# Optimization experiments

Measured on AMD Instinct MI355X. Metric: run time of the kernel, lower is better.

The kernel has to match this reference:

```python
import jax, jax.numpy as jnp
import numpy as np

NUM_CLASSES = 20
NUM_ANCHORS = 3
STRIDES = (8, 16, 32)
FMP = (320, 160, 80)
TOPK = 100
CONF_THRESH = 0.01
NMS_THRESH = 0.5
ANCHOR_SIZE = np.array([[12, 16], [19, 36], [40, 28], [36, 75], [76, 55], [72, 146],
                        [142, 110], [192, 243], [459, 401]], dtype=np.float32).reshape(3, NUM_ANCHORS, 2)


def make_anchors(level):
    h = w = FMP[level]
    ys, xs = jnp.meshgrid(jnp.arange(h, dtype=jnp.float32), jnp.arange(w, dtype=jnp.float32), indexing='ij')
    xy = jnp.stack([xs, ys], axis=-1).reshape(-1, 1, 2) + 0.5            # [HW,1,2] grid centers
    xy = jnp.broadcast_to(xy, (h * w, NUM_ANCHORS, 2))
    wh = jnp.broadcast_to(jnp.asarray(ANCHOR_SIZE[level]), (h * w, NUM_ANCHORS, 2))
    return jnp.concatenate([xy, wh], axis=-1).reshape(-1, 4)             # [HW*A, 4]


def level_topk(obj, cls, reg, level):
    C = NUM_CLASSES
    # [1, ch, H, W] -> [H*W*A, ch_per_anchor], matching permute(1,2,0).view(-1, .)
    obj = obj[0].transpose(1, 2, 0).reshape(-1, 1)
    cls = cls[0].transpose(1, 2, 0).reshape(-1, C)
    reg = reg[0].transpose(1, 2, 0).reshape(-1, 4)
    anchors = make_anchors(level)
    # decode: ctr = (sigmoid(txy)*3 - 1.5 + grid) * stride ; wh = exp(twh) * anchor_wh
    ctr = (jax.nn.sigmoid(reg[:, :2]) * 3.0 - 1.5 + anchors[:, :2]) * STRIDES[level]
    wh = jnp.exp(reg[:, 2:]) * anchors[:, 2:]
    boxes = jnp.concatenate([ctr - 0.5 * wh, ctr + 0.5 * wh], axis=-1)   # [N, 4] xyxy
    scores = (jax.nn.sigmoid(obj) * jax.nn.sigmoid(cls)).reshape(-1)     # [N*C]
    top_s, top_i = jax.lax.top_k(scores, TOPK)
    anchor_idx = top_i // C
    labels = top_i % C
    return top_s, labels, boxes[anchor_idx], top_s > CONF_THRESH


def nms_fixed(boxes, scores, labels, valid):
    # class-aware greedy NMS on a fixed candidate set; suppressed entries get score 0 / keep False
    K = scores.shape[0]
    order = jnp.argsort(-scores)
    b, s, l, v = boxes[order], scores[order], labels[order], valid[order]
    areas = (b[:, 2] - b[:, 0]) * (b[:, 3] - b[:, 1])
    xx1 = jnp.maximum(b[:, None, 0], b[None, :, 0])
    yy1 = jnp.maximum(b[:, None, 1], b[None, :, 1])
    xx2 = jnp.minimum(b[:, None, 2], b[None, :, 2])
    yy2 = jnp.minimum(b[:, None, 3], b[None, :, 3])
    inter = jnp.maximum(1e-10, xx2 - xx1) * jnp.maximum(1e-10, yy2 - yy1)
    iou = inter / (areas[:, None] + areas[None, :] - inter)
    sup_mat = (iou > NMS_THRESH) & (l[:, None] == l[None, :])            # per-class suppression
    idx = jnp.arange(K)

    def body(i, state):
        suppressed, keep = state
        is_kept = jnp.logical_and(jnp.logical_not(suppressed[i]), v[i])
        keep = keep.at[i].set(is_kept)
        suppressed = suppressed | (is_kept & sup_mat[i] & (idx > i))
        return suppressed, keep

    _, keep = jax.lax.fori_loop(0, K, body, (jnp.zeros(K, bool), jnp.zeros(K, bool)))
    return b, s * keep.astype(s.dtype), l, keep


def setup_inputs() -> dict:
    key = jax.random.key(0)
    ks = jax.random.split(key, 9)
    shapes = {
        'obj0': (1, NUM_ANCHORS, 320, 320), 'cls0': (1, NUM_ANCHORS * NUM_CLASSES, 320, 320), 'reg0': (1, NUM_ANCHORS * 4, 320, 320),
        'obj1': (1, NUM_ANCHORS, 160, 160), 'cls1': (1, NUM_ANCHORS * NUM_CLASSES, 160, 160), 'reg1': (1, NUM_ANCHORS * 4, 160, 160),
        'obj2': (1, NUM_ANCHORS, 80, 80), 'cls2': (1, NUM_ANCHORS * NUM_CLASSES, 80, 80), 'reg2': (1, NUM_ANCHORS * 4, 80, 80),
    }
    return {name: jax.random.normal(k, shp, dtype=jnp.float32)
            for k, (name, shp) in zip(ks, shapes.items())}


def reference(obj0, cls0, reg0, obj1, cls1, reg1, obj2, cls2, reg2):
    levels = [(obj0, cls0, reg0), (obj1, cls1, reg1), (obj2, cls2, reg2)]
    parts = [level_topk(o, c, r, i) for i, (o, c, r) in enumerate(levels)]
    scores = jnp.concatenate([p[0] for p in parts])
    labels = jnp.concatenate([p[1] for p in parts])
    boxes = jnp.concatenate([p[2] for p in parts])
    valid = jnp.concatenate([p[3] for p in parts])
    return nms_fixed(boxes, scores, labels, valid)  # (bboxes[300,4], scores[300], labels[300], keep[300])
```

## Files before the change

### kernel.cpp

```cpp
#include <hip/hip_runtime.h>
#include <stdint.h>

typedef unsigned int u32;
typedef unsigned long long u64;

#define TOPK 100
#define CAP 4096
#define NB 512
#define BINBASE 32000u
#define KAB_BLOCKS 394

__device__ const float ANC[3][3][2] = {
  {{12.f,16.f},{19.f,36.f},{40.f,28.f}},
  {{36.f,75.f},{76.f,55.f},{72.f,146.f}},
  {{142.f,110.f},{192.f,243.f},{459.f,401.f}}
};

__device__ __forceinline__ float sigmoidf_(float x) {
  if (x >= 0.f) return 1.f / (1.f + expf(-x));
  float e = expf(x);
  return e / (1.f + e);
}

__device__ __forceinline__ float fcomp(const float4& v, int q) {
  switch (q) {
    case 0: return v.x;
    case 1: return v.y;
    case 2: return v.z;
    default: return v.w;
  }
}

__global__ __launch_bounds__(256) void kA_scan(
    const float* __restrict__ obj0, const float* __restrict__ cls0,
    const float* __restrict__ obj1, const float* __restrict__ cls1,
    const float* __restrict__ obj2, const float* __restrict__ cls2,
    u32* __restrict__ hist, float* __restrict__ amax)
{
  __shared__ u32 h[NB];
  int tid = threadIdx.x;
  h[tid] = 0; h[tid + 256] = 0;
  __syncthreads();

  int b = blockIdx.x;
  const float *obj, *cls; int P, L, abase; u32 task;
  if (b < 300)      { L=0; obj=obj0; cls=cls0; P=102400; abase=0;      task=(u32)(b*256+tid); }
  else if (b < 375) { L=1; obj=obj1; cls=cls1; P=25600;  abase=307200; task=(u32)((b-300)*256+tid); }
  else              { L=2; obj=obj2; cls=cls2; P=6400;   abase=384000; task=(u32)((b-375)*256+tid); }
  int tpa = P >> 2;
  bool valid = task < (u32)(3*tpa);

  if (valid) {
    int a = (int)(task / (u32)tpa), rem = (int)(task % (u32)tpa);
    int p0 = rem * 4;
    float4 o4 = *(const float4*)(obj + a*P + p0);
    const float* cp = cls + (size_t)(a*20)*P + p0;
    float4 cv[20];
    #pragma unroll
    for (int k = 0; k < 20; ++k) cv[k] = *(const float4*)(cp + (size_t)k*P);
    float4 cm = cv[0];
    #pragma unroll
    for (int k = 1; k < 20; ++k) {
      cm.x = fmaxf(cm.x, cv[k].x); cm.y = fmaxf(cm.y, cv[k].y);
      cm.z = fmaxf(cm.z, cv[k].z); cm.w = fmaxf(cm.w, cv[k].w);
    }
    float4 am4;
    am4.x = sigmoidf_(o4.x) * sigmoidf_(cm.x);
    am4.y = sigmoidf_(o4.y) * sigmoidf_(cm.y);
    am4.z = sigmoidf_(o4.z) * sigmoidf_(cm.z);
    am4.w = sigmoidf_(o4.w) * sigmoidf_(cm.w);
    *(float4*)(amax + abase + a*P + p0) = am4;
    #pragma unroll
    for (int q = 0; q < 4; ++q) {
      u32 bt = __float_as_uint(fcomp(am4, q));
      if (bt >= (BINBASE << 15)) {
        u32 bin = (bt >> 15) - BINBASE;
        if (bin < NB) atomicAdd(&h[bin], 1u);
      }
    }
  }
  __syncthreads();
  if (h[tid])       atomicAdd(&hist[L*NB + tid],       h[tid]);
  if (h[tid + 256]) atomicAdd(&hist[L*NB + tid + 256], h[tid + 256]);
}

__global__ __launch_bounds__(256) void kB_collect(
    const float* __restrict__ obj0, const float* __restrict__ cls0,
    const float* __restrict__ obj1, const float* __restrict__ cls1,
    const float* __restrict__ obj2, const float* __restrict__ cls2,
    const float* __restrict__ amax, const u32* __restrict__ hist,
    u32* __restrict__ cnt, u64* __restrict__ cand)
{
  __shared__ u32 s[NB];
  __shared__ u32 sThr;
  int tid = threadIdx.x;
  int b = blockIdx.x;
  const float *obj, *cls; int P, L, abase; u32 task;
  if (b < 300)      { L=0; obj=obj0; cls=cls0; P=102400; abase=0;      task=(u32)(b*256+tid); }
  else if (b < 375) { L=1; obj=obj1; cls=cls1; P=25600;  abase=307200; task=(u32)((b-300)*256+tid); }
  else              { L=2; obj=obj2; cls=cls2; P=6400;   abase=384000; task=(u32)((b-375)*256+tid); }
  int tpa = P >> 2;
  bool valid = task < (u32)(3*tpa);

  s[tid] = hist[L*NB + tid]; s[tid + 256] = hist[L*NB + tid + 256];
  __syncthreads();
  for (int off = 1; off < NB; off <<= 1) {
    u32 v0 = s[tid]       + ((tid + off < NB)       ? s[tid + off]       : 0u);
    u32 v1 = s[tid + 256] + ((tid + 256 + off < NB) ? s[tid + 256 + off] : 0u);
    __syncthreads();
    s[tid] = v0; s[tid + 256] = v1;
    __syncthreads();
  }
  if (tid == 0 && s[0] < TOPK) sThr = BINBASE << 15;
  {
    int i0 = tid, i1 = tid + 256;
    u32 a0 = s[i0], n0 = (i0 + 1 < NB) ? s[i0 + 1] : 0u;
    if (a0 >= TOPK && n0 < TOPK) sThr = (BINBASE + (u32)i0) << 15;
    u32 a1 = s[i1], n1 = (i1 + 1 < NB) ? s[i1 + 1] : 0u;
    if (a1 >= TOPK && n1 < TOPK) sThr = (BINBASE + (u32)i1) << 15;
  }
  __syncthreads();
  u32 thr = sThr;

  if (valid) {
    int a = (int)(task / (u32)tpa), rem = (int)(task % (u32)tpa);
    int p0 = rem * 4;
    float4 am4 = *(const float4*)(amax + abase + a*P + p0);
    bool any = (__float_as_uint(am4.x) >= thr) | (__float_as_uint(am4.y) >= thr) |
               (__float_as_uint(am4.z) >= thr) | (__float_as_uint(am4.w) >= thr);
    if (any) {
      float4 o4 = *(const float4*)(obj + a*P + p0);
      const float* cp = cls + (size_t)(a*20)*P + p0;
      float4 cv[20];
      #pragma unroll
      for (int k = 0; k < 20; ++k) cv[k] = *(const float4*)(cp + (size_t)k*P);
      #pragma unroll
      for (int q = 0; q < 4; ++q) {
        if (__float_as_uint(fcomp(am4, q)) >= thr) {
          float so = sigmoidf_(fcomp(o4, q));
          int p = p0 + q;
          #pragma unroll
          for (int k = 0; k < 20; ++k) {
            float sc = so * sigmoidf_(fcomp(cv[k], q));
            u32 bits = __float_as_uint(sc);
            if (bits >= thr) {
              u32 pos = atomicAdd(&cnt[L], 1u);
              u32 idx = (u32)(p*60 + a*20 + k);
              if (pos < CAP) cand[L*CAP + pos] = ((u64)bits << 32) | (u64)(0x00FFFFFFu - idx);
            }
          }
        }
      }
    }
  }
}

__global__ __launch_bounds__(256) void kC1_select(
    const float* __restrict__ reg0, const float* __restrict__ reg1, const float* __restrict__ reg2,
    const u64* __restrict__ cand, const u32* __restrict__ cnt,
    u64* __restrict__ selg, float* __restrict__ boxg, float* __restrict__ scg,
    int* __restrict__ lbg, int* __restrict__ vdg)
{
  __shared__ u64 keys[CAP + 4];
  __shared__ u64 selL[TOPK];
  int tid = threadIdx.x;
  int L = blockIdx.x;

  if (tid < TOPK) selL[tid] = 0ull;
  __syncthreads();

  u32 n = cnt[L]; if (n > CAP) n = CAP;
  u32 n4 = (n + 3u) & ~3u;
  for (u32 j = (u32)tid; j < n; j += 256) keys[j] = cand[L*CAP + j];
  if (tid < 4 && n + (u32)tid < n4) keys[n + tid] = 0ull;
  __syncthreads();

  for (u32 j = (u32)tid; j < n; j += 256) {
    u64 kk = keys[j]; int r = 0;
    for (u32 t = 0; t < n4; t += 4) {
      u64 k0 = keys[t], k1 = keys[t+1], k2 = keys[t+2], k3 = keys[t+3];
      r += (k0 > kk) ? 1 : 0; r += (k1 > kk) ? 1 : 0;
      r += (k2 > kk) ? 1 : 0; r += (k3 > kk) ? 1 : 0;
    }
    if (r < TOPK) selL[r] = kk;
  }
  __syncthreads();

  if (tid < TOPK) {
    const float* reg; int Pq, W, stride;
    if (L == 0)      { reg = reg0; Pq = 102400; W = 320; stride = 8; }
    else if (L == 1) { reg = reg1; Pq = 25600;  W = 160; stride = 16; }
    else             { reg = reg2; Pq = 6400;   W = 80;  stride = 32; }
    int g = L*TOPK + tid;
    u64 key = selL[tid];
    selg[g] = key;
    if (key == 0) {
      scg[g] = 0.f; lbg[g] = 0; vdg[g] = 0;
      boxg[g*4+0] = boxg[g*4+1] = boxg[g*4+2] = boxg[g*4+3] = 0.f;
    } else {
      float score = __uint_as_float((u32)(key >> 32));
      u32 i = 0x00FFFFFFu - (u32)(key & 0xFFFFFFFFull);
      int c = (int)(i % 60u), p = (int)(i / 60u);
      int aa = c / 20, k = c % 20;
      int x = p % W, y = p / W;
      float tx = reg[(aa*4+0)*Pq + p], ty = reg[(aa*4+1)*Pq + p];
      float tw = reg[(aa*4+2)*Pq + p], th = reg[(aa*4+3)*Pq + p];
      float cx = (sigmoidf_(tx)*3.f - 1.5f + (float)x + 0.5f) * (float)stride;
      float cy = (sigmoidf_(ty)*3.f - 1.5f + (float)y + 0.5f) * (float)stride;
      float bw = expf(tw) * ANC[L][aa][0];
      float bh = expf(th) * ANC[L][aa][1];
      scg[g] = score; lbg[g] = k; vdg[g] = (score > 0.01f) ? 1 : 0;
      boxg[g*4+0] = cx - 0.5f*bw; boxg[g*4+1] = cy - 0.5f*bh;
      boxg[g*4+2] = cx + 0.5f*bw; boxg[g*4+3] = cy + 0.5f*bh;
    }
  }
}

__global__ __launch_bounds__(1024) void kC2_nms(
    const u64* __restrict__ selg, const float* __restrict__ boxg,
    const float* __restrict__ scg, const int* __restrict__ lbg, const int* __restrict__ vdg,
    float* __restrict__ out)
{
  extern __shared__ uint8_t smem[];
  u64*    mat   = (u64*)(smem);
  float4* ibox4 = (float4*)(smem + 12000);
  float2* iml2  = (float2*)(smem + 16800);
  float*  x1s   = (float*)(smem + 19200);
  float*  y1s   = (float*)(smem + 20400);
  float*  x2s   = (float*)(smem + 21600);
  float*  y2s   = (float*)(smem + 22800);
  float*  sc2   = (float*)(smem + 24000);
  int*    lb2   = (int*)(smem + 25200);
  int*    vd2   = (int*)(smem + 26400);
  u64*    rowAny= (u64*)(smem + 27600);
  u64*    km    = (u64*)(smem + 27648);
  float*  ars   = (float*)(smem + 27696);
  u64*    selAll= (u64*)(smem + 28896);

  int tid = threadIdx.x;
  if (tid < 300) selAll[tid] = selg[tid];
  __syncthreads();

  if (tid < 300) {
    int Lm = tid / TOPK, rr = tid % TOPK;
    u64 kk = selAll[tid];
    int rank = rr;
    #pragma unroll
    for (int Lo = 0; Lo < 3; ++Lo) {
      if (Lo == Lm) continue;
      const u64* arr = selAll + Lo*TOPK;
      bool ge = (Lo < Lm);
      int lo = 0;
      #pragma unroll
      for (int st = 64; st > 0; st >>= 1) {
        int nxt = lo + st;
        if (nxt <= TOPK) {
          u64 v = arr[nxt - 1];
          bool pred = ge ? (v >= kk) : (v > kk);
          if (pred) lo = nxt;
        }
      }
      rank += lo;
    }
    float4 bb = *(const float4*)(boxg + tid*4);
    float x1 = bb.x, y1 = bb.y, x2 = bb.z, y2 = bb.w;
    float ar = (x2 - x1) * (y2 - y1);
    ibox4[rank] = make_float4(x1, y1, x2, y2);
    iml2[rank]  = make_float2(ar, (float)lbg[tid]);
    x1s[rank] = x1; y1s[rank] = y1; x2s[rank] = x2; y2s[rank] = y2; ars[rank] = ar;
    sc2[rank] = scg[tid]; lb2[rank] = lbg[tid]; vd2[rank] = vdg[tid];
  }
  __syncthreads();

  {
    int wave = tid >> 6, lane = tid & 63;
    if (wave < 15) {
      int w = (wave >= 10) ? 4 : (wave >= 6) ? 3 : (wave >= 3) ? 2 : (wave >= 1) ? 1 : 0;
      int ns = w + 1;
      int stripe = wave - ((w*(w+1)) >> 1);
      int j = w*64 + lane;
      bool jv = j < 300;
      float jx1=0.f, jy1=0.f, jx2=0.f, jy2=0.f, jar=0.f; float jlb=-1.f;
      if (jv) { jx1=x1s[j]; jy1=y1s[j]; jx2=x2s[j]; jy2=y2s[j]; jar=ars[j]; jlb=(float)lb2[j]; }
      int ilim = (w+1)*64; if (ilim > 300) ilim = 300;
      #pragma unroll 2
      for (int i = stripe; i < ilim; i += ns) {
        float4 B = ibox4[i];
        float2 M = iml2[i];
        float xx1 = fmaxf(B.x, jx1), yy1 = fmaxf(B.y, jy1);
        float xx2 = fminf(B.z, jx2), yy2 = fminf(B.w, jy2);
        float inter = fmaxf(1e-10f, xx2-xx1) * fmaxf(1e-10f, yy2-yy1);
        float iou = inter / (M.x + jar - inter);
        bool pred = jv && (iou > 0.5f) && (M.y == jlb);
        u64 m = __ballot(pred);
        if (lane == 0) mat[i*5 + w] = m;
      }
    }
  }
  __syncthreads();

  {
    bool flag = false;
    if (tid < 300) {
      int c = tid >> 6, bq = tid & 63;
      u64 acc = mat[tid*5 + c] & ((bq == 63) ? 0ull : (~0ull << (bq + 1)));
      for (int w = c + 1; w < 5; ++w) acc |= mat[tid*5 + w];
      flag = (acc != 0ull);
    }
    u64 bal = __ballot(flag);
    if ((tid & 63) == 0 && (tid >> 6) < 5) rowAny[tid >> 6] = bal;
  }
  __syncthreads();

  if (tid < 64) {
    int lane = tid;
    u64 vm[5];
    #pragma unroll
    for (int c = 0; c < 5; ++c) {
      int j = c*64 + lane;
      vm[c] = __ballot((j < 300) && (vd2[j] != 0));
    }
    u64 ra[5];
    #pragma unroll
    for (int c = 0; c < 5; ++c) ra[c] = rowAny[c];
    u64 S[5] = {0,0,0,0,0};
    #pragma unroll
    for (int c = 0; c < 5; ++c) {
      u64 kbits = 0;
      int lim = (c == 4) ? 44 : 64;
      for (int t = 0; t < lim; ++t) {
        u64 kept = ((~(S[c] >> t)) & (vm[c] >> t)) & 1ull;
        kbits |= kept << t;
        if (kept & ((ra[c] >> t) & 1ull)) {
          int i = c*64 + t;
          #pragma unroll
          for (int w = 0; w < 5; ++w)
            if (w >= c) S[w] |= mat[i*5 + w];
        }
      }
      if (lane == 0) km[c] = kbits;
    }
  }
  __syncthreads();

  if (tid < 300) {
    float kf = (float)((km[tid >> 6] >> (tid & 63)) & 1ull);
    float4 bq = ibox4[tid];
    out[tid*4+0] = bq.x; out[tid*4+1] = bq.y;
    out[tid*4+2] = bq.z; out[tid*4+3] = bq.w;
    out[1200+tid] = sc2[tid] * kf;
    out[1500+tid] = (float)lb2[tid];
    out[1800+tid] = kf;
  }
}

extern "C" void kernel_launch(void* const* d_in, const int* in_sizes, int n_in,
                              void* d_out, int out_size, void* d_ws, size_t ws_size,
                              hipStream_t stream) {
  const float* obj0 = (const float*)d_in[0];
  const float* cls0 = (const float*)d_in[1];
  const float* reg0 = (const float*)d_in[2];
  const float* obj1 = (const float*)d_in[3];
  const float* cls1 = (const float*)d_in[4];
  const float* reg1 = (const float*)d_in[5];
  const float* obj2 = (const float*)d_in[6];
  const float* cls2 = (const float*)d_in[7];
  const float* reg2 = (const float*)d_in[8];
  float* out = (float*)d_out;

  uint8_t* ws = (uint8_t*)d_ws;
  u32*   hist = (u32*)(ws + 0);
  u32*   cnt  = (u32*)(ws + 6144);
  u64*   cand = (u64*)(ws + 8192);
  float* amax = (float*)(ws + 106496);
  u64*   selg = (u64*)(ws + 106496);
  float* boxg = (float*)(ws + 108896);
  float* scg  = (float*)(ws + 113696);
  int*   lbg  = (int*)(ws + 114896);
  int*   vdg  = (int*)(ws + 116096);

  (void)hipMemsetAsync(ws, 0, 6160, stream);

  kA_scan<<<dim3(KAB_BLOCKS), dim3(256), 0, stream>>>(
      obj0, cls0, obj1, cls1, obj2, cls2, hist, amax);
  kB_collect<<<dim3(KAB_BLOCKS), dim3(256), 0, stream>>>(
      obj0, cls0, obj1, cls1, obj2, cls2, amax, hist, cnt, cand);
  kC1_select<<<dim3(3), dim3(256), 0, stream>>>(
      reg0, reg1, reg2, cand, cnt, selg, boxg, scg, lbg, vdg);
  kC2_nms<<<dim3(1), dim3(1024), 31744, stream>>>(
      selg, boxg, scg, lbg, vdg, out);
}
```

Measured before the change: 157.3 us.

## Fuse scan, collect and select into one cooperative kernel with grid syncs

Merges the histogram scan, candidate collection and per-level top-k selection into a single cooperative launch that uses grid-wide syncs in place of kernel boundaries. The amax array is no longer stored and reloaded because it stays in registers across the sync. The workspace memset is replaced by zeroing inside block 0. The costs being removed are launch gaps and the extra global round trip, paid for with three grid barriers and a larger shared-memory footprint per block, which could limit residency.

```diff
diff --git a/kernel.cpp b/kernel.cpp
--- a/kernel.cpp
+++ b/kernel.cpp
@@ -1,5 +1,8 @@
 #include <hip/hip_runtime.h>
+#include <hip/hip_cooperative_groups.h>
 #include <stdint.h>
+
+namespace cg = cooperative_groups;
 
 typedef unsigned int u32;
 typedef unsigned long long u64;
@@ -31,28 +34,44 @@
   }
 }
 
-__global__ __launch_bounds__(256) void kA_scan(
-    const float* __restrict__ obj0, const float* __restrict__ cls0,
-    const float* __restrict__ obj1, const float* __restrict__ cls1,
-    const float* __restrict__ obj2, const float* __restrict__ cls2,
-    u32* __restrict__ hist, float* __restrict__ amax)
+__global__ __launch_bounds__(256) void kF_scan_collect_select(
+    const float* __restrict__ obj0, const float* __restrict__ cls0, const float* __restrict__ reg0,
+    const float* __restrict__ obj1, const float* __restrict__ cls1, const float* __restrict__ reg1,
+    const float* __restrict__ obj2, const float* __restrict__ cls2, const float* __restrict__ reg2,
+    u32* __restrict__ hist, u32* __restrict__ cnt, u64* __restrict__ cand,
+    u64* __restrict__ selg, float* __restrict__ boxg, float* __restrict__ scg,
+    int* __restrict__ lbg, int* __restrict__ vdg)
 {
-  __shared__ u32 h[NB];
+  cg::grid_group grid = cg::this_grid();
+  extern __shared__ uint8_t smem[];
+  u32* h = (u32*)smem;
+  u64* keys = (u64*)smem;
+  __shared__ u64 selL[TOPK];
+  __shared__ u32 sThr;
+
   int tid = threadIdx.x;
-  h[tid] = 0; h[tid + 256] = 0;
-  __syncthreads();
-
   int b = blockIdx.x;
-  const float *obj, *cls; int P, L, abase; u32 task;
-  if (b < 300)      { L=0; obj=obj0; cls=cls0; P=102400; abase=0;      task=(u32)(b*256+tid); }
-  else if (b < 375) { L=1; obj=obj1; cls=cls1; P=25600;  abase=307200; task=(u32)((b-300)*256+tid); }
-  else              { L=2; obj=obj2; cls=cls2; P=6400;   abase=384000; task=(u32)((b-375)*256+tid); }
+
+  if (b == 0) {
+    for (int i = tid; i < 3*NB; i += 256) hist[i] = 0u;
+    if (tid < 3) cnt[tid] = 0u;
+  }
+
+  h[tid] = 0u; h[tid + 256] = 0u;
+  __syncthreads();
+
+  const float *obj, *cls; int P, L; u32 task;
+  if (b < 300)      { L=0; obj=obj0; cls=cls0; P=102400; task=(u32)(b*256+tid); }
+  else if (b < 375) { L=1; obj=obj1; cls=cls1; P=25600;  task=(u32)((b-300)*256+tid); }
+  else              { L=2; obj=obj2; cls=cls2; P=6400;   task=(u32)((b-375)*256+tid); }
   int tpa = P >> 2;
   bool valid = task < (u32)(3*tpa);
 
+  int a = 0, p0 = 0;
+  float4 am4 = make_float4(0.f, 0.f, 0.f, 0.f);
   if (valid) {
-    int a = (int)(task / (u32)tpa), rem = (int)(task % (u32)tpa);
-    int p0 = rem * 4;
+    a = (int)(task / (u32)tpa);
+    p0 = (int)(task % (u32)tpa) * 4;
     float4 o4 = *(const float4*)(obj + a*P + p0);
     const float* cp = cls + (size_t)(a*20)*P + p0;
     float4 cv[20];
@@ -64,12 +83,10 @@
       cm.x = fmaxf(cm.x, cv[k].x); cm.y = fmaxf(cm.y, cv[k].y);
       cm.z = fmaxf(cm.z, cv[k].z); cm.w = fmaxf(cm.w, cv[k].w);
     }
-    float4 am4;
     am4.x = sigmoidf_(o4.x) * sigmoidf_(cm.x);
     am4.y = sigmoidf_(o4.y) * sigmoidf_(cm.y);
     am4.z = sigmoidf_(o4.z) * sigmoidf_(cm.z);
     am4.w = sigmoidf_(o4.w) * sigmoidf_(cm.w);
-    *(float4*)(amax + abase + a*P + p0) = am4;
     #pragma unroll
     for (int q = 0; q < 4; ++q) {
       u32 bt = __float_as_uint(fcomp(am4, q));
@@ -80,28 +97,13 @@
     }
   }
   __syncthreads();
+  grid.sync();
+
   if (h[tid])       atomicAdd(&hist[L*NB + tid],       h[tid]);
   if (h[tid + 256]) atomicAdd(&hist[L*NB + tid + 256], h[tid + 256]);
-}
-
-__global__ __launch_bounds__(256) void kB_collect(
-    const float* __restrict__ obj0, const float* __restrict__ cls0,
-    const float* __restrict__ obj1, const float* __restrict__ cls1,
-    const float* __restrict__ obj2, const float* __restrict__ cls2,
-    const float* __restrict__ amax, const u32* __restrict__ hist,
-    u32* __restrict__ cnt, u64* __restrict__ cand)
-{
-  __shared__ u32 s[NB];
-  __shared__ u32 sThr;
-  int tid = threadIdx.x;
-  int b = blockIdx.x;
-  const float *obj, *cls; int P, L, abase; u32 task;
-  if (b < 300)      { L=0; obj=obj0; cls=cls0; P=102400; abase=0;      task=(u32)(b*256+tid); }
-  else if (b < 375) { L=1; obj=obj1; cls=cls1; P=25600;  abase=307200; task=(u32)((b-300)*256+tid); }
-  else              { L=2; obj=obj2; cls=cls2; P=6400;   abase=384000; task=(u32)((b-375)*256+tid); }
-  int tpa = P >> 2;
-  bool valid = task < (u32)(3*tpa);
-
+  grid.sync();
+
+  u32* s = h;
   s[tid] = hist[L*NB + tid]; s[tid + 256] = hist[L*NB + tid + 256];
   __syncthreads();
   for (int off = 1; off < NB; off <<= 1) {
@@ -123,9 +125,6 @@
   u32 thr = sThr;
 
   if (valid) {
-    int a = (int)(task / (u32)tpa), rem = (int)(task % (u32)tpa);
-    int p0 = rem * 4;
-    float4 am4 = *(const float4*)(amax + abase + a*P + p0);
     bool any = (__float_as_uint(am4.x) >= thr) | (__float_as_uint(am4.y) >= thr) |
                (__float_as_uint(am4.z) >= thr) | (__float_as_uint(am4.w) >= thr);
     if (any) {
@@ -153,25 +152,17 @@
       }
     }
   }
-}
-
-__global__ __launch_bounds__(256) void kC1_select(
-    const float* __restrict__ reg0, const float* __restrict__ reg1, const float* __restrict__ reg2,
-    const u64* __restrict__ cand, const u32* __restrict__ cnt,
-    u64* __restrict__ selg, float* __restrict__ boxg, float* __restrict__ scg,
-    int* __restrict__ lbg, int* __restrict__ vdg)
-{
-  __shared__ u64 keys[CAP + 4];
-  __shared__ u64 selL[TOPK];
-  int tid = threadIdx.x;
-  int L = blockIdx.x;
-
+  grid.sync();
+
+  if (b >= 3) return;
+
+  int L1 = b;
   if (tid < TOPK) selL[tid] = 0ull;
   __syncthreads();
 
-  u32 n = cnt[L]; if (n > CAP) n = CAP;
+  u32 n = cnt[L1]; if (n > CAP) n = CAP;
   u32 n4 = (n + 3u) & ~3u;
-  for (u32 j = (u32)tid; j < n; j += 256) keys[j] = cand[L*CAP + j];
+  for (u32 j = (u32)tid; j < n; j += 256) keys[j] = cand[L1*CAP + j];
   if (tid < 4 && n + (u32)tid < n4) keys[n + tid] = 0ull;
   __syncthreads();
 
@@ -188,10 +179,10 @@
 
   if (tid < TOPK) {
     const float* reg; int Pq, W, stride;
-    if (L == 0)      { reg = reg0; Pq = 102400; W = 320; stride = 8; }
-    else if (L == 1) { reg = reg1; Pq = 25600;  W = 160; stride = 16; }
-    else             { reg = reg2; Pq = 6400;   W = 80;  stride = 32; }
-    int g = L*TOPK + tid;
+    if (L1 == 0)      { reg = reg0; Pq = 102400; W = 320; stride = 8; }
+    else if (L1 == 1) { reg = reg1; Pq = 25600;  W = 160; stride = 16; }
+    else              { reg = reg2; Pq = 6400;   W = 80;  stride = 32; }
+    int g = L1*TOPK + tid;
     u64 key = selL[tid];
     selg[g] = key;
     if (key == 0) {
@@ -207,8 +198,8 @@
       float tw = reg[(aa*4+2)*Pq + p], th = reg[(aa*4+3)*Pq + p];
       float cx = (sigmoidf_(tx)*3.f - 1.5f + (float)x + 0.5f) * (float)stride;
       float cy = (sigmoidf_(ty)*3.f - 1.5f + (float)y + 0.5f) * (float)stride;
-      float bw = expf(tw) * ANC[L][aa][0];
-      float bh = expf(th) * ANC[L][aa][1];
+      float bw = expf(tw) * ANC[L1][aa][0];
+      float bh = expf(th) * ANC[L1][aa][1];
       scg[g] = score; lbg[g] = k; vdg[g] = (score > 0.01f) ? 1 : 0;
       boxg[g*4+0] = cx - 0.5f*bw; boxg[g*4+1] = cy - 0.5f*bh;
       boxg[g*4+2] = cx + 0.5f*bw; boxg[g*4+3] = cy + 0.5f*bh;
@@ -372,21 +363,21 @@
   u32*   hist = (u32*)(ws + 0);
   u32*   cnt  = (u32*)(ws + 6144);
   u64*   cand = (u64*)(ws + 8192);
-  float* amax = (float*)(ws + 106496);
   u64*   selg = (u64*)(ws + 106496);
   float* boxg = (float*)(ws + 108896);
   float* scg  = (float*)(ws + 113696);
   int*   lbg  = (int*)(ws + 114896);
   int*   vdg  = (int*)(ws + 116096);
 
-  (void)hipMemsetAsync(ws, 0, 6160, stream);
-
-  kA_scan<<<dim3(KAB_BLOCKS), dim3(256), 0, stream>>>(
-      obj0, cls0, obj1, cls1, obj2, cls2, hist, amax);
-  kB_collect<<<dim3(KAB_BLOCKS), dim3(256), 0, stream>>>(
-      obj0, cls0, obj1, cls1, obj2, cls2, amax, hist, cnt, cand);
-  kC1_select<<<dim3(3), dim3(256), 0, stream>>>(
-      reg0, reg1, reg2, cand, cnt, selg, boxg, scg, lbg, vdg);
-  kC2_nms<<<dim3(1), dim3(1024), 31744, stream>>>(
-      selg, boxg, scg, lbg, vdg, out);
-}
+  void* args[] = {
+    (void*)&obj0, (void*)&cls0, (void*)&reg0,
+    (void*)&obj1, (void*)&cls1, (void*)&reg1,
+    (void*)&obj2, (void*)&cls2, (void*)&reg2,
+    (void*)&hist, (void*)&cnt, (void*)&cand,
+    (void*)&selg, (void*)&boxg, (void*)&scg, (void*)&lbg, (void*)&vdg
+  };
+  (void)hipLaunchCooperativeKernel((const void*)kF_scan_collect_select,
+      dim3(KAB_BLOCKS), dim3(256), args, 32832 , stream);
+
+  kC2_nms<<<dim3(1), dim3(1024), 31744, stream>>>(selg, boxg, scg, lbg, vdg, out);
+}
```

Result: slower. 278.6 us (+77.2%).
